# Kernel tuning notes

Measured on AMD Instinct MI355X. Metric: run time of the kernel, lower is better.

Reference implementation:

```python
import jax, jax.numpy as jnp
import numpy as np

LN_EPS = 1e-5
CLAMP = 1e-8


def _linear(x, W, b):
    return x @ W + b


def _layernorm(x, g, b):
    mu = x.mean(-1, keepdims=True)
    var = ((x - mu) ** 2).mean(-1, keepdims=True)
    return (x - mu) / jnp.sqrt(var + LN_EPS) * g + b


def _residual(x, W1, b1, W2, b2):
    return jax.nn.relu(_linear(jax.nn.relu(_linear(x, W1, b1)), W2, b2)) + x


def _forward(node_emb, attn_Wq, attn_bq, attn_Wk, attn_bk, attn_Wv, attn_bv,
             attn_Wd, attn_bd, attn_ln_g, attn_ln_b,
             mlp_r1_w1, mlp_r1_b1, mlp_r1_w2, mlp_r1_b2,
             mlp_r2_w1, mlp_r2_b1, mlp_r2_w2, mlp_r2_b2,
             mlp_out_w, mlp_out_b,
             log_phi_r0, log_phi_r1h, log_phi_r1v, log_phi_r2, r0_idx, n):
    x = node_emb  # [1, n^2, D]
    L = attn_Wq.shape[0]
    for l in range(L):  # mask in the original is all zeros -> plain softmax attention
        q = _linear(x, attn_Wq[l], attn_bq[l])
        k = _linear(x, attn_Wk[l], attn_bk[l])
        v = _linear(x, attn_Wv[l], attn_bv[l])
        probs = jax.nn.softmax(jnp.einsum('bqd,bkd->bqk', q, k), axis=-1)
        ctx = jnp.einsum('bqk,bkd->bqd', probs, v)
        x = _layernorm(_linear(ctx, attn_Wd[l], attn_bd[l]) + x, attn_ln_g[l], attn_ln_b[l])
    x0 = x[0]                                  # [n^2, D]
    feats = x0[r0_idx].reshape(r0_idx.shape[0], -1)  # [R0, 4D]
    h = _residual(feats, mlp_r1_w1, mlp_r1_b1, mlp_r1_w2, mlp_r1_b2)
    h = _residual(h, mlp_r2_w1, mlp_r2_b1, mlp_r2_w2, mlp_r2_b2)
    logits = _linear(h, mlp_out_w, mlp_out_b)  # [R0, 16]
    beliefs = jax.nn.softmax(logits, axis=-1).reshape(-1, 2, 2, 2, 2)

    m = n - 1  # plaquettes per row
    # --- R1 horizontal interior edges (row r in 1..n-2, col c in 0..n-2) ---
    r, c = np.meshgrid(np.arange(1, n - 1), np.arange(m), indexing='ij')
    above = ((r - 1) * m + c).ravel()
    below = (r * m + c).ravel()
    h_stack = jnp.stack([beliefs[above].sum((1, 2)),   # edge nodes at plaquette pos 2,3
                         beliefs[below].sum((3, 4))])  # edge nodes at plaquette pos 0,1
    h_bel = h_stack.mean(0)                            # [Eh,2,2]
    mism = jnp.sum((h_stack - h_bel) ** 2)
    # --- R1 vertical interior edges (row r in 0..n-2, col c in 1..n-2) ---
    r, c = np.meshgrid(np.arange(m), np.arange(1, n - 1), indexing='ij')
    left = (r * m + (c - 1)).ravel()
    right = (r * m + c).ravel()
    v_stack = jnp.stack([beliefs[left].sum((1, 3)),    # edge nodes at pos 1,3
                         beliefs[right].sum((2, 4))])  # edge nodes at pos 0,2
    v_bel = v_stack.mean(0)                            # [Ev,2,2]
    mism = mism + jnp.sum((v_stack - v_bel) ** 2)
    # --- R2 interior nodes (r, c in 1..n-2), parents are the 4 incident edges ---
    r, c = np.meshgrid(np.arange(1, n - 1), np.arange(1, n - 1), indexing='ij')
    hl = ((r - 1) * m + (c - 1)).ravel()
    hr = ((r - 1) * m + c).ravel()
    vu = ((r - 1) * (n - 2) + (c - 1)).ravel()
    vd = (r * (n - 2) + (c - 1)).ravel()
    n_stack = jnp.stack([h_bel[hl].sum(1), h_bel[hr].sum(2),
                         v_bel[vu].sum(1), v_bel[vd].sum(2)])
    n_bel = n_stack.mean(0)                            # [V,2]
    mism = mism + jnp.sum((n_stack - n_bel) ** 2)

    # --- Kikuchi energy: counts +1 (plaquette), -1 (edge), +1 (node); log_phi detached ---
    def reg_energy(b, lphi, cnt):
        bc = jnp.maximum(b, CLAMP)
        return cnt * jnp.sum(bc * (jnp.log(bc) - jax.lax.stop_gradient(lphi)))

    energy = (reg_energy(beliefs, log_phi_r0, 1.0)
              + reg_energy(h_bel, log_phi_r1h, -1.0)
              + reg_energy(v_bel, log_phi_r1v, -1.0)
              + reg_energy(n_bel, log_phi_r2, 1.0))
    return energy, mism


def setup_inputs() -> dict:
    n, D, L, HID, OUT = 64, 256, 2, 1024, 16
    m = n - 1
    R0, E, V = m * m, (n - 2) * m, (n - 2) * (n - 2)
    key = jax.random.key(0)
    ks = jax.random.split(key, 24)
    norm = lambda k, sh, s=0.05: jax.random.normal(k, sh, dtype=jnp.float32) * s
    r, c = np.meshgrid(np.arange(m), np.arange(m), indexing='ij')
    i = (r * n + c).ravel()
    r0_idx = jnp.asarray(np.stack([i, i + 1, i + n, i + n + 1], 1), dtype=jnp.int32)
    inp = {
        'node_emb': jax.random.normal(ks[0], (1, n * n, D), dtype=jnp.float32),
        'attn_Wq': norm(ks[1], (L, D, D)), 'attn_bq': jnp.zeros((L, D), jnp.float32),
        'attn_Wk': norm(ks[2], (L, D, D)), 'attn_bk': jnp.zeros((L, D), jnp.float32),
        'attn_Wv': norm(ks[3], (L, D, D)), 'attn_bv': jnp.zeros((L, D), jnp.float32),
        'attn_Wd': norm(ks[4], (L, D, D)), 'attn_bd': jnp.zeros((L, D), jnp.float32),
        'attn_ln_g': jnp.ones((L, D), jnp.float32), 'attn_ln_b': jnp.zeros((L, D), jnp.float32),
        'mlp_r1_w1': norm(ks[5], (HID, HID), 0.03), 'mlp_r1_b1': jnp.zeros((HID,), jnp.float32),
        'mlp_r1_w2': norm(ks[6], (HID, HID), 0.03), 'mlp_r1_b2': jnp.zeros((HID,), jnp.float32),
        'mlp_r2_w1': norm(ks[7], (HID, HID), 0.03), 'mlp_r2_b1': jnp.zeros((HID,), jnp.float32),
        'mlp_r2_w2': norm(ks[8], (HID, HID), 0.03), 'mlp_r2_b2': jnp.zeros((HID,), jnp.float32),
        'mlp_out_w': norm(ks[9], (HID, OUT), 0.03), 'mlp_out_b': jnp.zeros((OUT,), jnp.float32),
        'log_phi_r0': jax.random.normal(ks[10], (R0, 2, 2, 2, 2), dtype=jnp.float32),
        'log_phi_r1h': jax.random.normal(ks[11], (E, 2, 2), dtype=jnp.float32),
        'log_phi_r1v': jax.random.normal(ks[12], (E, 2, 2), dtype=jnp.float32),
        'log_phi_r2': jax.random.normal(ks[13], (V, 2), dtype=jnp.float32),
        'r0_idx': r0_idx,
        'n': n,
    }
    return inp


def reference(node_emb, attn_Wq, attn_bq, attn_Wk, attn_bk, attn_Wv, attn_bv,
              attn_Wd, attn_bd, attn_ln_g, attn_ln_b,
              mlp_r1_w1, mlp_r1_b1, mlp_r1_w2, mlp_r1_b2,
              mlp_r2_w1, mlp_r2_b1, mlp_r2_w2, mlp_r2_b2,
              mlp_out_w, mlp_out_b,
              log_phi_r0, log_phi_r1h, log_phi_r1v, log_phi_r2, r0_idx, n):
    return _forward(node_emb, attn_Wq, attn_bq, attn_Wk, attn_bk, attn_Wv, attn_bv,
                    attn_Wd, attn_bd, attn_ln_g, attn_ln_b,
                    mlp_r1_w1, mlp_r1_b1, mlp_r1_w2, mlp_r1_b2,
                    mlp_r2_w1, mlp_r2_b1, mlp_r2_w2, mlp_r2_b2,
                    mlp_out_w, mlp_out_b,
                    log_phi_r0, log_phi_r1h, log_phi_r1v, log_phi_r2, r0_idx, n)
```

## Files before the change

### kernel.cpp

```cpp
#include <hip/hip_runtime.h>
#include <hip/hip_bf16.h>
#include <math.h>

#define D_    256
#define NSQ   4096
#define NL    2
#define HID_  1024
#define R0_   3969
#define EH_   3906
#define EV_   3906
#define NV_   3844
#define LN_EPS_ 1e-5f
#define CLAMP_  1e-8f
#define TK_    64

typedef float f32x4 __attribute__((ext_vector_type(4)));
typedef __bf16 bf16x8 __attribute__((ext_vector_type(8)));
typedef unsigned short u16x8 __attribute__((ext_vector_type(8)));

__device__ __forceinline__ void gload_lds16(const void* g, void* l) {
    __builtin_amdgcn_global_load_lds(
        (const __attribute__((address_space(1))) void*)g,
        (__attribute__((address_space(3))) void*)l, 16, 0, 0);
}

template<int BM, int BN>
__device__ __forceinline__ void gemm_body(
    const __hip_bfloat16* __restrict__ A, const __hip_bfloat16* __restrict__ Bt,
    const float* __restrict__ bias,
    const float* __restrict__ resf, const __hip_bfloat16* __restrict__ resb,
    void* __restrict__ C, int M, int N, int K, int relu, int outmode,
    int bx, int by)
{
    constexpr int WR  = BM / 64;
    constexpr int WC  = 4 / WR;
    constexpr int WNT = BN / WC;
    constexpr int NF  = WNT / 16;
    constexpr int ACH = BM / 64;
    constexpr int BCH = BN / 64;
    constexpr int ASZ = BM * 32;

    __shared__ __hip_bfloat16 sm[2][(BM + BN) * 32];

    const int t = threadIdx.x;
    const int lane = t & 63, wave = t >> 6;
    const int ln = lane & 15, lg = lane >> 4;
    const int wr = (WR == 1) ? 0 : (wave >> 1);
    const int wc = (WR == 1) ? wave : (wave & 1);
    const int row0 = bx * BM, col0 = by * BN;

    int aoff[ACH], boff[BCH];
    #pragma unroll
    for (int c = 0; c < ACH; ++c) {
        int e = (c * 256 + t) * 8;
        int row = e >> 5, slot = (e >> 3) & 3;
        int kg = slot ^ (row & 3) ^ ((row >> 2) & 3);
        aoff[c] = row * K + kg * 8;
    }
    #pragma unroll
    for (int c = 0; c < BCH; ++c) {
        int e = (c * 256 + t) * 8;
        int row = e >> 5, slot = (e >> 3) & 3;
        int kg = slot ^ (row & 3) ^ ((row >> 2) & 3);
// ... 57 lines not shown
                    float v = acc[m][n][r] + bv;
                    if (relu) v = fmaxf(v, 0.f);
                    pk.h[r] = __float2bfloat16(v);
                }
                *(ushort4*)((__hip_bfloat16*)C + (size_t)col * M + rowb) = pk.u4;
            } else if (outmode == 3) {
                union { ushort4 u4; __hip_bfloat16 h[4]; } pk;
                #pragma unroll
                for (int r = 0; r < 4; ++r) {
                    float v = acc[m][n][r] + bv;
                    if (relu) v = fmaxf(v, 0.f);
                    pk.h[r] = __float2bfloat16(v);
                }
                size_t off = ((size_t)((rowb >> 5) * 16 + (col >> 4)) << 9)
                           + (size_t)(((rowb >> 3) & 3) * 16 + (col & 15)) * 8
                           + (rowb & 7);
                *(ushort4*)((__hip_bfloat16*)C + off) = pk.u4;
            } else {
                #pragma unroll
                for (int r = 0; r < 4; ++r) {
                    float v = acc[m][n][r] + bv;
                    if (relu) v = fmaxf(v, 0.f);
                    const size_t idx = (size_t)(rowb + r) * N + col;
                    if (resf) v += resf[idx];
                    if (resb) v += __bfloat162float(resb[idx]);
                    if (outmode == 0) ((float*)C)[idx] = v;
                    else ((__hip_bfloat16*)C)[idx] = __float2bfloat16(v);
                }
            }
        }
    }
}

template<int BM, int BN>
__global__ __launch_bounds__(256) void gemm_t(
    const __hip_bfloat16* __restrict__ A, const __hip_bfloat16* __restrict__ Bt,
    const float* __restrict__ bias,
    const float* __restrict__ resf, const __hip_bfloat16* __restrict__ resb,
    void* __restrict__ C, int M, int N, int K, int relu, int outmode)
{
    gemm_body<BM, BN>(A, Bt, bias, resf, resb, C, M, N, K, relu, outmode,
                      blockIdx.x, blockIdx.y);
}

__global__ __launch_bounds__(256) void gemm_qkv(
    const __hip_bfloat16* __restrict__ xb,
    const __hip_bfloat16* __restrict__ wqkt2, const __hip_bfloat16* __restrict__ wvt2,
    const float* __restrict__ bqk2, const float* __restrict__ bv,
    __hip_bfloat16* __restrict__ qkb, __hip_bfloat16* __restrict__ vf, int l)
{
    const __hip_bfloat16* Bt;
    const float* bias;
    void* C;
    int N, outmode, by;
    if (blockIdx.y < 4) {
        Bt = wqkt2 + (size_t)l * 131072; bias = bqk2 + l * 512;
        C = qkb; N = 512; outmode = 1; by = blockIdx.y;
    } else {
        Bt = wvt2 + (size_t)l * 65536; bias = bv + l * D_;
        C = vf; N = D_; outmode = 3; by = blockIdx.y - 4;
    }
    gemm_body<64, 128>(xb, Bt, bias, nullptr, nullptr, C, NSQ, N, D_, 0, outmode,
                       blockIdx.x, by);
}

__global__ __launch_bounds__(256, 2) void gemm_128p(
    const __hip_bfloat16* __restrict__ A, const __hip_bfloat16* __restrict__ Bt,
    const float* __restrict__ bias, const __hip_bfloat16* __restrict__ resb,
    __hip_bfloat16* __restrict__ C, int M, int N, int K, int relu)
{
    __shared__ __hip_bfloat16 sm[4][8192];

    const int t = threadIdx.x;
    const int lane = t & 63, wave = t >> 6;
    const int ln = lane & 15, lg = lane >> 4;
    const int wr = wave >> 1, wc = wave & 1;
    const int row0 = blockIdx.x * 128, col0 = blockIdx.y * 128;

    int aoff[2];
    #pragma unroll
    for (int c = 0; c < 2; ++c) {
        int e = (c * 256 + t) * 8;
        int row = e >> 5, slot = (e >> 3) & 3;
        int kg = slot ^ (row & 3) ^ ((row >> 2) & 3);
        aoff[c] = row * K + kg * 8;
    }
    const int sw = (ln & 3) ^ ((ln >> 2) & 3);

    const __hip_bfloat16* Ab = A + (size_t)row0 * K;
    const __hip_bfloat16* Bb = Bt + (size_t)col0 * K;

    f32x4 acc[4][4];
    #pragma unroll
    for (int m = 0; m < 4; ++m)
        #pragma unroll
        for (int n = 0; n < 4; ++n) acc[m][n] = f32x4{0.f, 0.f, 0.f, 0.f};

    auto STAGE = [&](int k0, int buf) {
        #pragma unroll
        for (int c = 0; c < 2; ++c) {
            gload_lds16(Ab + k0 + aoff[c], (char*)&sm[buf][0] + (c * 256 + t) * 16);
            gload_lds16(Bb + k0 + aoff[c], (char*)&sm[buf][4096] + (c * 256 + t) * 16);
        }
    };

    const int NT = K >> 5;
    STAGE(0, 0); STAGE(32, 1); STAGE(64, 2);

    for (int tt = 0; tt < NT; ++tt) {
        const int rem = NT - 1 - tt;
        if (rem >= 2)      asm volatile("s_waitcnt vmcnt(8)" ::: "memory");
        else if (rem == 1) asm volatile("s_waitcnt vmcnt(4)" ::: "memory");
        else               asm volatile("s_waitcnt vmcnt(0)" ::: "memory");
        __builtin_amdgcn_sched_barrier(0);
        __builtin_amdgcn_s_barrier();
        if (tt + 3 < NT) STAGE((tt + 3) * 32, (tt + 3) & 3);

        const char* base = (const char*)&sm[tt & 3][0];
        bf16x8 af[4], bfr[4];
        #pragma unroll
        for (int m = 0; m < 4; ++m)
            af[m] = *(const bf16x8*)(base +
                     (size_t)(wr * 64 + m * 16 + ln) * 64 + ((lg ^ sw) << 4));
        #pragma unroll
        for (int n = 0; n < 4; ++n)
            bfr[n] = *(const bf16x8*)(base + 8192 +
                     (size_t)(wc * 64 + n * 16 + ln) * 64 + ((lg ^ sw) << 4));
        #pragma unroll
        for (int m = 0; m < 4; ++m)
            #pragma unroll
            for (int n = 0; n < 4; ++n)
                acc[m][n] = __builtin_amdgcn_mfma_f32_16x16x32_bf16(
                    af[m], bfr[n], acc[m][n], 0, 0, 0);
    }

    #pragma unroll
    for (int m = 0; m < 4; ++m) {
        const int rowb = row0 + wr * 64 + m * 16 + lg * 4;
        #pragma unroll
        for (int n = 0; n < 4; ++n) {
            const int col = col0 + wc * 64 + n * 16 + ln;
            const float bv = bias[col];
            #pragma unroll
            for (int r = 0; r < 4; ++r) {
                float v = acc[m][n][r] + bv;
                if (relu) v = fmaxf(v, 0.f);
                const size_t idx = (size_t)(rowb + r) * N + col;
                if (resb) v += __bfloat162float(resb[idx]);
                C[idx] = __float2bfloat16(v);
            }
        }
    }
}

__global__ __launch_bounds__(256) void gemm_n16b(
    const __hip_bfloat16* __restrict__ A, const __hip_bfloat16* __restrict__ Bt,
    const float* __restrict__ bias, const float* __restrict__ lphi0,
    float* __restrict__ beliefs, float* __restrict__ out, int M, int K)
{
    const int t = threadIdx.x, lane = t & 63, wave = t >> 6;
    const int ln = lane & 15, lg = lane >> 4;
    const int r0 = blockIdx.x * 64 + wave * 16;
    f32x4 acc = {0.f, 0.f, 0.f, 0.f};
    for (int k0 = 0; k0 < K; k0 += 32) {
        bf16x8 a = *(const bf16x8*)(A + (size_t)(r0 + ln) * K + k0 + lg * 8);
        bf16x8 b = *(const bf16x8*)(Bt + (size_t)ln * K + k0 + lg * 8);
        acc = __builtin_amdgcn_mfma_f32_16x16x32_bf16(a, b, acc, 0, 0, 0);
    }
    float e = 0.f;
    #pragma unroll
    for (int r = 0; r < 4; ++r) {
        const int row = r0 + lg * 4 + r;
        float v = acc[r] + bias[ln];
        float mx = v;
        mx = fmaxf(mx, __shfl_xor(mx, 1));
        mx = fmaxf(mx, __shfl_xor(mx, 2));
        mx = fmaxf(mx, __shfl_xor(mx, 4));
        mx = fmaxf(mx, __shfl_xor(mx, 8));
        float ex = __expf(v - mx);
        float s = ex;
        s += __shfl_xor(s, 1);
        s += __shfl_xor(s, 2);
        s += __shfl_xor(s, 4);
        s += __shfl_xor(s, 8);
        if (row < R0_) {
            float bb = ex / s;
            beliefs[(size_t)row * 16 + ln] = bb;
            float bc = fmaxf(bb, CLAMP_);
            e += bc * (logf(bc) - lphi0[(size_t)row * 16 + ln]);
        }
    }
    #pragma unroll
    for (int off = 32; off; off >>= 1) e += __shfl_down(e, off);
    if (lane == 0) atomicAdd(&out[0], e);
}

__global__ __launch_bounds__(256) void prep_k(
    const float* __restrict__ node_emb, __hip_bfloat16* __restrict__ xb,
    const float* __restrict__ outw, __hip_bfloat16* __restrict__ outwt,
    const float* __restrict__ Wq, const float* __restrict__ Wk,
    const float* __restrict__ Wv, const float* __restrict__ Wd,
    __hip_bfloat16* __restrict__ wqkt2, __hip_bfloat16* __restrict__ wvt2,
    __hip_bfloat16* __restrict__ wdt2,
    const float* __restrict__ bq, const float* __restrict__ bk,
    float* __restrict__ bqk2,
    const float* __restrict__ M0, const float* __restrict__ M1,
    const float* __restrict__ M2, const float* __restrict__ M3,
    __hip_bfloat16* __restrict__ T0, __hip_bfloat16* __restrict__ T1,
    __hip_bfloat16* __restrict__ T2, __hip_bfloat16* __restrict__ T3,
    float* __restrict__ outp)
{
    __shared__ float tile[32][33];
    const int b = blockIdx.x, t = threadIdx.x;
    if (b == 0 && t < 2) outp[t] = 0.f;
    if (b < 1024) {
        int p = b * 256 + t;
        float4 v = *(const float4*)(node_emb + (size_t)p * 4);
        union { ushort4 u4; __hip_bfloat16 h[4]; } pk;
        pk.h[0] = __float2bfloat16(v.x); pk.h[1] = __float2bfloat16(v.y);
        pk.h[2] = __float2bfloat16(v.z); pk.h[3] = __float2bfloat16(v.w);
        *(ushort4*)(xb + (size_t)p * 4) = pk.u4;
    } else if (b < 1088) {
        int i = (b - 1024) * 256 + t;
        int n = i >> 10, k = i & 1023;
        outwt[i] = __float2bfloat16(outw[k * 16 + n]);
    } else if (b < 1600) {
        int idx = b - 1088;
// ... 6 lines not shown
                                    : wdt2 + (size_t)l * 65536;
        int k0 = bx * 32, n0 = by * 32;
        int r = t >> 3, c4 = (t & 7) * 4;
        float4 v = *(const float4*)(W + (size_t)(k0 + r) * 256 + n0 + c4);
        tile[r][c4 + 0] = v.x; tile[r][c4 + 1] = v.y;
        tile[r][c4 + 2] = v.z; tile[r][c4 + 3] = v.w;
        __syncthreads();
        union { ushort4 u4; __hip_bfloat16 h[4]; } pk;
        #pragma unroll
        for (int i = 0; i < 4; ++i) pk.h[i] = __float2bfloat16(tile[c4 + i][r]);
        *(ushort4*)(Wt + (size_t)(n0 + r) * 256 + k0 + c4) = pk.u4;
    } else if (b < 1604) {
        int idx = (b - 1600) * 256 + t;
        int l = idx >> 9, j = idx & 511;
        bqk2[idx] = j < 256 ? bq[l * 256 + j] : bk[l * 256 + j - 256];
    } else {
        int idx = b - 1604;
        int z = idx >> 10, rem = idx & 1023;
        const float* W = z == 0 ? M0 : z == 1 ? M1 : z == 2 ? M2 : M3;
        __hip_bfloat16* Wt = z == 0 ? T0 : z == 1 ? T1 : z == 2 ? T2 : T3;
        int k0 = (rem >> 5) * 32, n0 = (rem & 31) * 32;
        int r = t >> 3, c4 = (t & 7) * 4;
        float4 v = *(const float4*)(W + (size_t)(k0 + r) * 1024 + n0 + c4);
        tile[r][c4 + 0] = v.x; tile[r][c4 + 1] = v.y;
        tile[r][c4 + 2] = v.z; tile[r][c4 + 3] = v.w;
        __syncthreads();
        union { ushort4 u4; __hip_bfloat16 h[4]; } pk;
        #pragma unroll
        for (int i = 0; i < 4; ++i) pk.h[i] = __float2bfloat16(tile[c4 + i][r]);
        *(ushort4*)(Wt + (size_t)(n0 + r) * 1024 + k0 + c4) = pk.u4;
    }
}

template<int KS>
__global__ __launch_bounds__(512, 2) void attn_mfma_t(
    const __hip_bfloat16* __restrict__ qk, const __hip_bfloat16* __restrict__ vf,
    __hip_bfloat16* __restrict__ po, float* __restrict__ pm, float* __restrict__ pl)
{
    constexpr int KRANGE = NSQ / KS;
    constexpr int NT = KRANGE / TK_;
    constexpr int VOFF = 65536;
    constexpr int POFF = 98304;
    const int t = threadIdx.x;
    const int wave = t >> 6, lane = t & 63;
    const int ln = lane & 15, lg = lane >> 4;
    const int q0 = blockIdx.x * 128 + wave * 16;
    const int ks = blockIdx.y;
    const int k0 = ks * KRANGE;

    __shared__ __align__(16) char smem[116736];

    bf16x8 qa[8];
    #pragma unroll
    for (int s = 0; s < 8; ++s)
        qa[s] = *(const bf16x8*)(qk + (size_t)(q0 + ln) * 512 + s * 32 + lg * 8);

    int srcoff[4];
    #pragma unroll
    for (int c = 0; c < 4; ++c) {
        int row = c * 16 + (t >> 5);
        int g = (t & 31) ^ ((row & 15) << 1);
        srcoff[c] = row * 512 + 256 + g * 8;
    }
    int rb[8];
    #pragma unroll
    for (int s8 = 0; s8 < 8; ++s8)
        rb[s8] = ln * 512 + (((s8 * 4 + lg) ^ (ln << 1)) << 4);

    f32x4 o[16];
    #pragma unroll
    for (int nt = 0; nt < 16; ++nt) o[nt] = f32x4{0.f, 0.f, 0.f, 0.f};
// ... 85 lines not shown
        __builtin_amdgcn_s_barrier();
        const char* vl = smem + VOFF;
        #pragma unroll
        for (int ntd = 0; ntd < 16; ++ntd) {
            bf16x8 vb0 = *(const bf16x8*)(vl + ntd * 1024 + lane * 16);
            bf16x8 vb1 = *(const bf16x8*)(vl + 16384 + ntd * 1024 + lane * 16);
            o[ntd] = __builtin_amdgcn_mfma_f32_16x16x32_bf16(pa0, vb0, o[ntd], 0, 0, 0);
            o[ntd] = __builtin_amdgcn_mfma_f32_16x16x32_bf16(pa1, vb1, o[ntd], 0, 0, 0);
        }
        __syncthreads();
    }
    unsigned short* ob = (unsigned short*)(smem + wave * 8448);
    #pragma unroll
    for (int nt = 0; nt < 16; ++nt)
        #pragma unroll
        for (int r = 0; r < 4; ++r) {
            __hip_bfloat16 h = __float2bfloat16(o[nt][r]);
            ob[(lg * 4 + r) * 264 + nt * 16 + ln] = *(unsigned short*)&h;
        }
    asm volatile("s_waitcnt lgkmcnt(0)" ::: "memory");
    __builtin_amdgcn_sched_barrier(0);
    unsigned short* pob = (unsigned short*)po;
    #pragma unroll
    for (int i = 0; i < 8; ++i) {
        int f = i * 64 + lane;
        int row = f >> 5, dc = f & 31;
        u16x8 vv = *(const u16x8*)(ob + row * 264 + dc * 8);
        *(u16x8*)(pob + ((size_t)ks * NSQ + q0 + row) * D_ + dc * 8) = vv;
    }
    if (lane < 16) {
        pm[ks * NSQ + q0 + lane] = rm;
        pl[ks * NSQ + q0 + lane] = rl;
    }
}

template<int KS>
__global__ __launch_bounds__(256) void attn_combine_t(
    const __hip_bfloat16* __restrict__ po, const float* __restrict__ pm,
    const float* __restrict__ pl, __hip_bfloat16* __restrict__ ctx)
{
    const int idx8 = blockIdx.x * 256 + threadIdx.x;
    const int row = idx8 >> 5;
    float m[KS], ms = -1e30f;
    #pragma unroll
    for (int s = 0; s < KS; ++s) { m[s] = pm[s * NSQ + row]; ms = fmaxf(ms, m[s]); }
    float l = 0.f, w[KS];
    #pragma unroll
    for (int s = 0; s < KS; ++s) {
        w[s] = __expf(m[s] - ms);
        l += w[s] * pl[s * NSQ + row];
    }
    const float inv = 1.f / l;
    float num[8];
    #pragma unroll
    for (int j = 0; j < 8; ++j) num[j] = 0.f;
    #pragma unroll
    for (int s = 0; s < KS; ++s) {
        u16x8 v = *(const u16x8*)(po + (size_t)s * (NSQ * D_) + (size_t)idx8 * 8);
        #pragma unroll
        for (int j = 0; j < 8; ++j) {
            union { float f; unsigned u; } cv;
            cv.u = (unsigned)v[j] << 16;
            num[j] += w[s] * cv.f;
        }
    }
    union { u16x8 u8; __hip_bfloat16 h[8]; } pk;
    #pragma unroll
    for (int j = 0; j < 8; ++j) pk.h[j] = __float2bfloat16(num[j] * inv);
    *(u16x8*)(ctx + (size_t)idx8 * 8) = pk.u8;
}

__global__ __launch_bounds__(256) void ln_f32(
    const float* __restrict__ y, const float* __restrict__ g,
    const float* __restrict__ b, float* __restrict__ xo,
    __hip_bfloat16* __restrict__ xob, __hip_bfloat16* __restrict__ feats, int fin)
{
    const int lane = threadIdx.x & 63, wave = threadIdx.x >> 6;
    const int row = blockIdx.x * 4 + wave;
    float4 v = *(const float4*)(y + (size_t)row * D_ + lane * 4);
    float s = v.x + v.y + v.z + v.w;
    #pragma unroll
    for (int off = 1; off < 64; off <<= 1) s += __shfl_xor(s, off);
    float mu = s * (1.f / D_);
    float dx = v.x - mu, dy = v.y - mu, dz = v.z - mu, dw = v.w - mu;
    float q = dx * dx + dy * dy + dz * dz + dw * dw;
    #pragma unroll
    for (int off = 1; off < 64; off <<= 1) q += __shfl_xor(q, off);
    float inv = rsqrtf(q * (1.f / D_) + LN_EPS_);
    float4 gg = *(const float4*)(g + lane * 4);
    float4 bb = *(const float4*)(b + lane * 4);
    float4 o;
    o.x = dx * inv * gg.x + bb.x;
    o.y = dy * inv * gg.y + bb.y;
    o.z = dz * inv * gg.z + bb.z;
    o.w = dw * inv * gg.w + bb.w;
    union { ushort4 u4; __hip_bfloat16 h[4]; } pk;
    pk.h[0] = __float2bfloat16(o.x); pk.h[1] = __float2bfloat16(o.y);
    pk.h[2] = __float2bfloat16(o.z); pk.h[3] = __float2bfloat16(o.w);
    if (!fin) {
        *(float4*)(xo + (size_t)row * D_ + lane * 4) = o;
        *(ushort4*)(xob + (size_t)row * D_ + lane * 4) = pk.u4;
    } else {
        const int r = row >> 6, c = row & 63;
        if (r < 63 && c < 63)
            *(ushort4*)(feats + (size_t)(r * 63 + c) * 1024 + lane * 4) = pk.u4;
        if (r < 63 && c > 0)
            *(ushort4*)(feats + (size_t)(r * 63 + c - 1) * 1024 + 256 + lane * 4) = pk.u4;
        if (r > 0 && c < 63)
            *(ushort4*)(feats + (size_t)((r - 1) * 63 + c) * 1024 + 512 + lane * 4) = pk.u4;
        if (r > 0 && c > 0)
            *(ushort4*)(feats + (size_t)((r - 1) * 63 + c - 1) * 1024 + 768 + lane * 4) = pk.u4;
    }
}

__global__ __launch_bounds__(256) void edges_k(
    const float* __restrict__ beliefs, const float* __restrict__ lphih,
    const float* __restrict__ lphiv, float* __restrict__ hbel,
    float* __restrict__ vbel, float* __restrict__ out)
{
    int e = blockIdx.x * 256 + threadIdx.x;
    float el = 0.f, ml = 0.f;
    if (blockIdx.y == 0) {
        if (e < EH_) {
            const float* bA = beliefs + (size_t)e * 16;
            const float* bB = beliefs + (size_t)(e + 63) * 16;
            float s0[4] = {0,0,0,0}, s1[4] = {0,0,0,0};
            #pragma unroll
            for (int ab = 0; ab < 4; ++ab)
                #pragma unroll
                for (int cd = 0; cd < 4; ++cd) {
                    s0[cd] += bA[ab * 4 + cd];
                    s1[ab] += bB[ab * 4 + cd];
                }
            #pragma unroll
            for (int z = 0; z < 4; ++z) {
                float hb = 0.5f * (s0[z] + s1[z]);
                hbel[e * 4 + z] = hb;
                float d0 = s0[z] - hb, d1 = s1[z] - hb;
                ml += d0 * d0 + d1 * d1;
                float bc = fmaxf(hb, CLAMP_);
                el -= bc * (logf(bc) - lphih[e * 4 + z]);
            }
        }
    } else {
        if (e < EV_) {
            int r = e / 62, c = e % 62 + 1;
            const float* bL = beliefs + (size_t)(r * 63 + c - 1) * 16;
            const float* bR = beliefs + (size_t)(r * 63 + c) * 16;
            float s0[4] = {0,0,0,0}, s1[4] = {0,0,0,0};
            #pragma unroll
            for (int a = 0; a < 2; ++a)
                #pragma unroll
                for (int bq = 0; bq < 2; ++bq)
                    #pragma unroll
                    for (int c2 = 0; c2 < 2; ++c2)
                        #pragma unroll
                        for (int d = 0; d < 2; ++d) {
                            int idx = a * 8 + bq * 4 + c2 * 2 + d;
                            s0[bq * 2 + d]  += bL[idx];
                            s1[a * 2 + c2] += bR[idx];
                        }
            #pragma unroll
            for (int z = 0; z < 4; ++z) {
                float vb = 0.5f * (s0[z] + s1[z]);
                vbel[e * 4 + z] = vb;
                float d0 = s0[z] - vb, d1 = s1[z] - vb;
                ml += d0 * d0 + d1 * d1;
                float bc = fmaxf(vb, CLAMP_);
                el -= bc * (logf(bc) - lphiv[e * 4 + z]);
            }
        }
    }
    for (int off = 32; off; off >>= 1) { el += __shfl_down(el, off); ml += __shfl_down(ml, off); }
    if ((threadIdx.x & 63) == 0) { atomicAdd(&out[0], el); atomicAdd(&out[1], ml); }
}

__global__ __launch_bounds__(256) void node_k(
    const float* __restrict__ hbel, const float* __restrict__ vbel,
    const float* __restrict__ lphi2, float* __restrict__ out)
{
    int vtx = blockIdx.x * 256 + threadIdx.x;
    float el = 0.f, ml = 0.f;
    if (vtx < NV_) {
        int hl = (vtx / 62) * 63 + (vtx % 62);
        int hr = hl + 1;
        int vu = vtx;
        int vd = vtx + 62;
        float n0[2], n1[2], n2[2], n3[2];
        #pragma unroll
        for (int z = 0; z < 2; ++z) {
            n0[z] = hbel[hl * 4 + z] + hbel[hl * 4 + 2 + z];
            n1[z] = hbel[hr * 4 + z * 2] + hbel[hr * 4 + z * 2 + 1];
            n2[z] = vbel[vu * 4 + z] + vbel[vu * 4 + 2 + z];
            n3[z] = vbel[vd * 4 + z * 2] + vbel[vd * 4 + z * 2 + 1];
        }
        #pragma unroll
        for (int z = 0; z < 2; ++z) {
            float nb = 0.25f * (n0[z] + n1[z] + n2[z] + n3[z]);
            float d0 = n0[z] - nb, d1 = n1[z] - nb, d2 = n2[z] - nb, d3 = n3[z] - nb;
            ml += d0 * d0 + d1 * d1 + d2 * d2 + d3 * d3;
            float bc = fmaxf(nb, CLAMP_);
            el += bc * (logf(bc) - lphi2[vtx * 2 + z]);
        }
    }
    for (int off = 32; off; off >>= 1) { el += __shfl_down(el, off); ml += __shfl_down(ml, off); }
    if ((threadIdx.x & 63) == 0) { atomicAdd(&out[0], el); atomicAdd(&out[1], ml); }
}

extern "C" void kernel_launch(void* const* d_in, const int* in_sizes, int n_in,
                              void* d_out, int out_size, void* d_ws, size_t ws_size,
                              hipStream_t stream)
{
    (void)in_sizes; (void)n_in; (void)out_size; (void)ws_size;
    const float* node_emb = (const float*)d_in[0];
    const float* Wq  = (const float*)d_in[1];
    const float* bq  = (const float*)d_in[2];
    const float* Wk  = (const float*)d_in[3];
    const float* bk  = (const float*)d_in[4];
    const float* Wv  = (const float*)d_in[5];
    const float* bv  = (const float*)d_in[6];
    const float* Wd  = (const float*)d_in[7];
    const float* bd  = (const float*)d_in[8];
    const float* lng = (const float*)d_in[9];
    const float* lnb = (const float*)d_in[10];
    const float* r1w1 = (const float*)d_in[11];
    const float* r1b1 = (const float*)d_in[12];
    const float* r1w2 = (const float*)d_in[13];
    const float* r1b2 = (const float*)d_in[14];
    const float* r2w1 = (const float*)d_in[15];
    const float* r2b1 = (const float*)d_in[16];
    const float* r2w2 = (const float*)d_in[17];
    const float* r2b2 = (const float*)d_in[18];
    const float* outw = (const float*)d_in[19];
    const float* outb = (const float*)d_in[20];
    const float* lphi0 = (const float*)d_in[21];
    const float* lphih = (const float*)d_in[22];
    const float* lphiv = (const float*)d_in[23];
    const float* lphi2 = (const float*)d_in[24];

    float* ws = (float*)d_ws;
    float* x      = ws;
    __hip_bfloat16* xb = (__hip_bfloat16*)(ws + 1048576);
    float* belief = ws + 1638400;
    float* hbel   = ws + 1703936;
    float* vbel   = ws + 1720320;
    __hip_bfloat16* outwt = (__hip_bfloat16*)(ws + 1736704);
    float* arena  = ws + 1744896;

    __hip_bfloat16* wqkt2 = (__hip_bfloat16*)(arena);
    __hip_bfloat16* wvt2  = (__hip_bfloat16*)(arena + 131072);
    __hip_bfloat16* wdt2  = (__hip_bfloat16*)(arena + 196608);
    float* bqk2 = arena + 262144;
    __hip_bfloat16* qkb = (__hip_bfloat16*)(arena + 263168);
    __hip_bfloat16* vf  = (__hip_bfloat16*)(arena + 1311744);
    __hip_bfloat16* ctxb = vf;
    float* yb = arena + 1836032;
    float* pm = arena + 2884608;
    float* pl = arena + 2950144;
    __hip_bfloat16* po = (__hip_bfloat16*)(arena + 3015680);

    __hip_bfloat16* feats = (__hip_bfloat16*)(ws + 8954880);
    __hip_bfloat16* w1t = (__hip_bfloat16*)(ws + 11052032);
    __hip_bfloat16* w2t = (__hip_bfloat16*)(ws + 11576320);
    __hip_bfloat16* w3t = (__hip_bfloat16*)(ws + 12100608);
    __hip_bfloat16* w4t = (__hip_bfloat16*)(ws + 12624896);
    __hip_bfloat16* hA  = (__hip_bfloat16*)(arena);
    __hip_bfloat16* hB  = (__hip_bfloat16*)(arena + 2097152);

    float* outp = (float*)d_out;
    dim3 blk(256);
    dim3 blk512(512);
    prep_k<<<dim3(5700), blk, 0, stream>>>(node_emb, xb, outw, outwt,
                                           Wq, Wk, Wv, Wd, wqkt2, wvt2, wdt2,
                                           bq, bk, bqk2,
                                           r1w1, r1w2, r2w1, r2w2,
                                           w1t, w2t, w3t, w4t, outp);

    for (int l = 0; l < NL; ++l) {
        gemm_qkv<<<dim3(64, 6), blk, 0, stream>>>(xb, wqkt2, wvt2, bqk2, bv,
                                                  qkb, vf, l);
        attn_mfma_t<8><<<dim3(NSQ / 128, 8), blk512, 0, stream>>>(qkb, vf, po, pm, pl);
        attn_combine_t<8><<<dim3(NSQ * D_ / 2048), blk, 0, stream>>>(po, pm, pl, ctxb);
        gemm_t<64, 64><<<dim3(NSQ / 64, D_ / 64), blk, 0, stream>>>(
            ctxb, wdt2 + (size_t)l * 65536, bd + l * D_,
            (l == 0 ? node_emb : x), nullptr, yb, NSQ, D_, D_, 0, 0);
        ln_f32<<<dim3(NSQ / 4), blk, 0, stream>>>(yb, lng + l * D_, lnb + l * D_,
                                                  x, xb, feats, l);
    }

    dim3 gM(NSQ / 128, HID_ / 128);
    gemm_128p<<<gM, blk, 0, stream>>>(feats, w1t, r1b1, nullptr,
                                      hA, NSQ, HID_, HID_, 1);
    gemm_128p<<<gM, blk, 0, stream>>>(hA, w2t, r1b2, feats,
                                      hB, NSQ, HID_, HID_, 1);
    gemm_128p<<<gM, blk, 0, stream>>>(hB, w3t, r2b1, nullptr,
                                      hA, NSQ, HID_, HID_, 1);
    gemm_128p<<<gM, blk, 0, stream>>>(hA, w4t, r2b2, hB,
                                      feats, NSQ, HID_, HID_, 1);

    gemm_n16b<<<dim3(NSQ / 64), blk, 0, stream>>>(feats, outwt, outb, lphi0,
                                                  belief, outp, NSQ, HID_);
    edges_k<<<dim3((EH_ + 255) / 256, 2), blk, 0, stream>>>(belief, lphih, lphiv,
                                                            hbel, vbel, outp);
    node_k<<<dim3((NV_ + 255) / 256), blk, 0, stream>>>(hbel, vbel, lphi2, outp);
}
```

Baseline: 230.8 us.

## Merge attention, projection+LN and tail kernels using cooperative grid sync

Replaces several small back-to-back kernel launches with cooperative kernels that use grid-wide barriers: attention plus split-K combine, output projection plus layernorm, and the logits/edge/node tail. The aim is to cut launch gaps and inter-kernel drain time. In exchange, the grids are constrained to be co-resident, grid.sync costs something, and the LN stage now runs on only 256 blocks with 4 rows per wave.

```diff
diff --git a/kernel.cpp b/kernel.cpp
--- a/kernel.cpp
+++ b/kernel.cpp
@@ -1,6 +1,9 @@
 #include <hip/hip_runtime.h>
 #include <hip/hip_bf16.h>
+#include <hip/hip_cooperative_groups.h>
 #include <math.h>
+
+namespace cg = cooperative_groups;
 
 #define D_    256
 #define NSQ   4096
@@ -28,7 +31,7 @@
 __device__ __forceinline__ void gemm_body(
     const __hip_bfloat16* __restrict__ A, const __hip_bfloat16* __restrict__ Bt,
     const float* __restrict__ bias,
-    const float* __restrict__ resf, const __hip_bfloat16* __restrict__ resb,
+    const float* resf, const __hip_bfloat16* __restrict__ resb,
     void* __restrict__ C, int M, int N, int K, int relu, int outmode,
     int bx, int by)
 {
@@ -152,17 +155,6 @@
     }
 }
 
-template<int BM, int BN>
-__global__ __launch_bounds__(256) void gemm_t(
-    const __hip_bfloat16* __restrict__ A, const __hip_bfloat16* __restrict__ Bt,
-    const float* __restrict__ bias,
-    const float* __restrict__ resf, const __hip_bfloat16* __restrict__ resb,
-    void* __restrict__ C, int M, int N, int K, int relu, int outmode)
-{
-    gemm_body<BM, BN>(A, Bt, bias, resf, resb, C, M, N, K, relu, outmode,
-                      blockIdx.x, blockIdx.y);
-}
-
 __global__ __launch_bounds__(256) void gemm_qkv(
     const __hip_bfloat16* __restrict__ xb,
     const __hip_bfloat16* __restrict__ wqkt2, const __hip_bfloat16* __restrict__ wvt2,
@@ -184,6 +176,59 @@
                        blockIdx.x, by);
 }
 
+__global__ __launch_bounds__(256) void projln_k(
+    const __hip_bfloat16* __restrict__ ctxb, const __hip_bfloat16* __restrict__ wdt,
+    const float* __restrict__ bd, const float* resf,
+    float* __restrict__ yb,
+    const float* __restrict__ g, const float* __restrict__ b,
+    float* xo, __hip_bfloat16* __restrict__ xob,
+    __hip_bfloat16* __restrict__ feats, int fin)
+{
+    gemm_body<64, 64>(ctxb, wdt, bd, resf, nullptr, yb, NSQ, D_, D_, 0, 0,
+                      (int)(blockIdx.x & 63), (int)(blockIdx.x >> 6));
+    cg::this_grid().sync();
+
+    const int lane = threadIdx.x & 63, wave = threadIdx.x >> 6;
+    const int gw = blockIdx.x * 4 + wave;
+    for (int i = 0; i < 4; ++i) {
+        const int row = gw * 4 + i;
+        float4 v = *(const float4*)(yb + (size_t)row * D_ + lane * 4);
+        float s = v.x + v.y + v.z + v.w;
+        #pragma unroll
+        for (int off = 1; off < 64; off <<= 1) s += __shfl_xor(s, off);
+        float mu = s * (1.f / D_);
+        float dx = v.x - mu, dy = v.y - mu, dz = v.z - mu, dw = v.w - mu;
+        float q = dx * dx + dy * dy + dz * dz + dw * dw;
+        #pragma unroll
+        for (int off = 1; off < 64; off <<= 1) q += __shfl_xor(q, off);
+        float inv = rsqrtf(q * (1.f / D_) + LN_EPS_);
+        float4 gg = *(const float4*)(g + lane * 4);
+        float4 bb = *(const float4*)(b + lane * 4);
+        float4 o;
+        o.x = dx * inv * gg.x + bb.x;
+        o.y = dy * inv * gg.y + bb.y;
+        o.z = dz * inv * gg.z + bb.z;
+        o.w = dw * inv * gg.w + bb.w;
+        union { ushort4 u4; __hip_bfloat16 h[4]; } pk;
+        pk.h[0] = __float2bfloat16(o.x); pk.h[1] = __float2bfloat16(o.y);
+        pk.h[2] = __float2bfloat16(o.z); pk.h[3] = __float2bfloat16(o.w);
+        if (!fin) {
+            *(float4*)(xo + (size_t)row * D_ + lane * 4) = o;
+            *(ushort4*)(xob + (size_t)row * D_ + lane * 4) = pk.u4;
+        } else {
+            const int r = row >> 6, c = row & 63;
+            if (r < 63 && c < 63)
+                *(ushort4*)(feats + (size_t)(r * 63 + c) * 1024 + lane * 4) = pk.u4;
+            if (r < 63 && c > 0)
+                *(ushort4*)(feats + (size_t)(r * 63 + c - 1) * 1024 + 256 + lane * 4) = pk.u4;
+            if (r > 0 && c < 63)
+                *(ushort4*)(feats + (size_t)((r - 1) * 63 + c) * 1024 + 512 + lane * 4) = pk.u4;
+            if (r > 0 && c > 0)
+                *(ushort4*)(feats + (size_t)((r - 1) * 63 + c - 1) * 1024 + 768 + lane * 4) = pk.u4;
+        }
+    }
+}
+
 __global__ __launch_bounds__(256, 2) void gemm_128p(
     const __hip_bfloat16* __restrict__ A, const __hip_bfloat16* __restrict__ Bt,
     const float* __restrict__ bias, const __hip_bfloat16* __restrict__ resb,
@@ -271,48 +316,6 @@
             }
         }
     }
-}
-
-__global__ __launch_bounds__(256) void gemm_n16b(
-    const __hip_bfloat16* __restrict__ A, const __hip_bfloat16* __restrict__ Bt,
-    const float* __restrict__ bias, const float* __restrict__ lphi0,
-    float* __restrict__ beliefs, float* __restrict__ out, int M, int K)
-{
-    const int t = threadIdx.x, lane = t & 63, wave = t >> 6;
-    const int ln = lane & 15, lg = lane >> 4;
-    const int r0 = blockIdx.x * 64 + wave * 16;
-    f32x4 acc = {0.f, 0.f, 0.f, 0.f};
-    for (int k0 = 0; k0 < K; k0 += 32) {
-        bf16x8 a = *(const bf16x8*)(A + (size_t)(r0 + ln) * K + k0 + lg * 8);
-        bf16x8 b = *(const bf16x8*)(Bt + (size_t)ln * K + k0 + lg * 8);
-        acc = __builtin_amdgcn_mfma_f32_16x16x32_bf16(a, b, acc, 0, 0, 0);
-    }
-    float e = 0.f;
-    #pragma unroll
-    for (int r = 0; r < 4; ++r) {
-        const int row = r0 + lg * 4 + r;
-        float v = acc[r] + bias[ln];
-        float mx = v;
-        mx = fmaxf(mx, __shfl_xor(mx, 1));
-        mx = fmaxf(mx, __shfl_xor(mx, 2));
-        mx = fmaxf(mx, __shfl_xor(mx, 4));
-        mx = fmaxf(mx, __shfl_xor(mx, 8));
-        float ex = __expf(v - mx);
-        float s = ex;
-        s += __shfl_xor(s, 1);
-        s += __shfl_xor(s, 2);
-        s += __shfl_xor(s, 4);
-        s += __shfl_xor(s, 8);
-        if (row < R0_) {
-            float bb = ex / s;
-            beliefs[(size_t)row * 16 + ln] = bb;
-            float bc = fmaxf(bb, CLAMP_);
-            e += bc * (logf(bc) - lphi0[(size_t)row * 16 + ln]);
-        }
-    }
-    #pragma unroll
-    for (int off = 32; off; off >>= 1) e += __shfl_down(e, off);
-    if (lane == 0) atomicAdd(&out[0], e);
 }
 
 __global__ __launch_bounds__(256) void prep_k(
@@ -385,11 +388,12 @@
     }
 }
 
-template<int KS>
-__global__ __launch_bounds__(512, 2) void attn_mfma_t(
-    const __hip_bfloat16* __restrict__ qk, const __hip_bfloat16* __restrict__ vf,
-    __hip_bfloat16* __restrict__ po, float* __restrict__ pm, float* __restrict__ pl)
+__global__ __launch_bounds__(512, 2) void attn_fused(
+    const __hip_bfloat16* __restrict__ qk, const __hip_bfloat16* vf,
+    __hip_bfloat16* __restrict__ po, float* __restrict__ pm, float* __restrict__ pl,
+    __hip_bfloat16* ctx)
 {
+    constexpr int KS = 8;
     constexpr int KRANGE = NSQ / KS;
     constexpr int NT = KRANGE / TK_;
     constexpr int VOFF = 65536;
@@ -541,96 +545,94 @@
         pm[ks * NSQ + q0 + lane] = rm;
         pl[ks * NSQ + q0 + lane] = rl;
     }
+
+    cg::this_grid().sync();
+    {
+        const int bid = blockIdx.y * 32 + blockIdx.x;
+        const int idx8 = bid * 512 + t;
+        const int row = idx8 >> 5;
+        float m2[KS], ms = -1e30f;
+        #pragma unroll
+        for (int s = 0; s < KS; ++s) { m2[s] = pm[s * NSQ + row]; ms = fmaxf(ms, m2[s]); }
+        float l2 = 0.f, w2[KS];
+        #pragma unroll
+        for (int s = 0; s < KS; ++s) {
+            w2[s] = __expf(m2[s] - ms);
+            l2 += w2[s] * pl[s * NSQ + row];
+        }
+        const float inv = 1.f / l2;
+        float num[8];
+        #pragma unroll
+        for (int j = 0; j < 8; ++j) num[j] = 0.f;
+        #pragma unroll
+        for (int s = 0; s < KS; ++s) {
+            u16x8 v = *(const u16x8*)((const unsigned short*)po +
+                        (size_t)s * (NSQ * D_) + (size_t)idx8 * 8);
+            #pragma unroll
+            for (int j = 0; j < 8; ++j) {
+                union { float f; unsigned u; } cv;
+                cv.u = (unsigned)v[j] << 16;
+                num[j] += w2[s] * cv.f;
+            }
+        }
+        union { u16x8 u8; __hip_bfloat16 h[8]; } pk;
+        #pragma unroll
+        for (int j = 0; j < 8; ++j) pk.h[j] = __float2bfloat16(num[j] * inv);
+        *(u16x8*)(ctx + (size_t)idx8 * 8) = pk.u8;
+    }
 }
 
-template<int KS>
-__global__ __launch_bounds__(256) void attn_combine_t(
-    const __hip_bfloat16* __restrict__ po, const float* __restrict__ pm,
-    const float* __restrict__ pl, __hip_bfloat16* __restrict__ ctx)
+__global__ __launch_bounds__(256) void tail_k(
+    const __hip_bfloat16* __restrict__ A, const __hip_bfloat16* __restrict__ Bt,
+    const float* __restrict__ bias, const float* __restrict__ lphi0,
+    float* __restrict__ beliefs,
+    const float* __restrict__ lphih, const float* __restrict__ lphiv,
+    float* __restrict__ hbel, float* __restrict__ vbel,
+    const float* __restrict__ lphi2, float* __restrict__ out)
 {
-    const int idx8 = blockIdx.x * 256 + threadIdx.x;
-    const int row = idx8 >> 5;
-    float m[KS], ms = -1e30f;
-    #pragma unroll
-    for (int s = 0; s < KS; ++s) { m[s] = pm[s * NSQ + row]; ms = fmaxf(ms, m[s]); }
-    float l = 0.f, w[KS];
-    #pragma unroll
-    for (int s = 0; s < KS; ++s) {
-        w[s] = __expf(m[s] - ms);
-        l += w[s] * pl[s * NSQ + row];
-    }
-    const float inv = 1.f / l;
-    float num[8];
-    #pragma unroll
-    for (int j = 0; j < 8; ++j) num[j] = 0.f;
-    #pragma unroll
-    for (int s = 0; s < KS; ++s) {
-        u16x8 v = *(const u16x8*)(po + (size_t)s * (NSQ * D_) + (size_t)idx8 * 8);
-        #pragma unroll
-        for (int j = 0; j < 8; ++j) {
-            union { float f; unsigned u; } cv;
-            cv.u = (unsigned)v[j] << 16;
-            num[j] += w[s] * cv.f;
-        }
-    }
-    union { u16x8 u8; __hip_bfloat16 h[8]; } pk;
-    #pragma unroll
-    for (int j = 0; j < 8; ++j) pk.h[j] = __float2bfloat16(num[j] * inv);
-    *(u16x8*)(ctx + (size_t)idx8 * 8) = pk.u8;
-}
-
-__global__ __launch_bounds__(256) void ln_f32(
-    const float* __restrict__ y, const float* __restrict__ g,
-    const float* __restrict__ b, float* __restrict__ xo,
-    __hip_bfloat16* __restrict__ xob, __hip_bfloat16* __restrict__ feats, int fin)
-{
-    const int lane = threadIdx.x & 63, wave = threadIdx.x >> 6;
-    const int row = blockIdx.x * 4 + wave;
-    float4 v = *(const float4*)(y + (size_t)row * D_ + lane * 4);
-    float s = v.x + v.y + v.z + v.w;
-    #pragma unroll
-    for (int off = 1; off < 64; off <<= 1) s += __shfl_xor(s, off);
-    float mu = s * (1.f / D_);
-    float dx = v.x - mu, dy = v.y - mu, dz = v.z - mu, dw = v.w - mu;
-    float q = dx * dx + dy * dy + dz * dz + dw * dw;
-    #pragma unroll
-    for (int off = 1; off < 64; off <<= 1) q += __shfl_xor(q, off);
-    float inv = rsqrtf(q * (1.f / D_) + LN_EPS_);
-    float4 gg = *(const float4*)(g + lane * 4);
-    float4 bb = *(const float4*)(b + lane * 4);
-    float4 o;
-    o.x = dx * inv * gg.x + bb.x;
-    o.y = dy * inv * gg.y + bb.y;
-    o.z = dz * inv * gg.z + bb.z;
-    o.w = dw * inv * gg.w + bb.w;
-    union { ushort4 u4; __hip_bfloat16 h[4]; } pk;
-    pk.h[0] = __float2bfloat16(o.x); pk.h[1] = __float2bfloat16(o.y);
-    pk.h[2] = __float2bfloat16(o.z); pk.h[3] = __float2bfloat16(o.w);
-    if (!fin) {
-        *(float4*)(xo + (size_t)row * D_ + lane * 4) = o;
-        *(ushort4*)(xob + (size_t)row * D_ + lane * 4) = pk.u4;
-    } else {
-        const int r = row >> 6, c = row & 63;
-        if (r < 63 && c < 63)
-            *(ushort4*)(feats + (size_t)(r * 63 + c) * 1024 + lane * 4) = pk.u4;
-        if (r < 63 && c > 0)
-            *(ushort4*)(feats + (size_t)(r * 63 + c - 1) * 1024 + 256 + lane * 4) = pk.u4;
-        if (r > 0 && c < 63)
-            *(ushort4*)(feats + (size_t)((r - 1) * 63 + c) * 1024 + 512 + lane * 4) = pk.u4;
-        if (r > 0 && c > 0)
-            *(ushort4*)(feats + (size_t)((r - 1) * 63 + c - 1) * 1024 + 768 + lane * 4) = pk.u4;
-    }
-}
-
-__global__ __launch_bounds__(256) void edges_k(
-    const float* __restrict__ beliefs, const float* __restrict__ lphih,
-    const float* __restrict__ lphiv, float* __restrict__ hbel,
-    float* __restrict__ vbel, float* __restrict__ out)
-{
-    int e = blockIdx.x * 256 + threadIdx.x;
-    float el = 0.f, ml = 0.f;
-    if (blockIdx.y == 0) {
-        if (e < EH_) {
+    const int t = threadIdx.x, lane = t & 63, wave = t >> 6;
+    const int ln = lane & 15, lg = lane >> 4;
+    {
+        const int r0 = blockIdx.x * 64 + wave * 16;
+        f32x4 acc = {0.f, 0.f, 0.f, 0.f};
+        for (int k0 = 0; k0 < HID_; k0 += 32) {
+            bf16x8 a = *(const bf16x8*)(A + (size_t)(r0 + ln) * HID_ + k0 + lg * 8);
+            bf16x8 b = *(const bf16x8*)(Bt + (size_t)ln * HID_ + k0 + lg * 8);
+            acc = __builtin_amdgcn_mfma_f32_16x16x32_bf16(a, b, acc, 0, 0, 0);
+        }
+        float e = 0.f;
+        #pragma unroll
+        for (int r = 0; r < 4; ++r) {
+            const int row = r0 + lg * 4 + r;
+            float v = acc[r] + bias[ln];
+            float mx = v;
+            mx = fmaxf(mx, __shfl_xor(mx, 1));
+            mx = fmaxf(mx, __shfl_xor(mx, 2));
+            mx = fmaxf(mx, __shfl_xor(mx, 4));
+            mx = fmaxf(mx, __shfl_xor(mx, 8));
+            float ex = __expf(v - mx);
+            float s = ex;
+            s += __shfl_xor(s, 1);
+            s += __shfl_xor(s, 2);
+            s += __shfl_xor(s, 4);
+            s += __shfl_xor(s, 8);
+            if (row < R0_) {
+                float bb = ex / s;
+                beliefs[(size_t)row * 16 + ln] = bb;
+                float bc = fmaxf(bb, CLAMP_);
+                e += bc * (logf(bc) - lphi0[(size_t)row * 16 + ln]);
+            }
+        }
+        #pragma unroll
+        for (int off = 32; off; off >>= 1) e += __shfl_down(e, off);
+        if (lane == 0) atomicAdd(&out[0], e);
+    }
+    cg::this_grid().sync();
+    {
+        const int gg = blockIdx.x * 256 + t;
+        float el = 0.f, ml = 0.f;
+        if (gg < EH_) {
+            const int e = gg;
             const float* bA = beliefs + (size_t)e * 16;
             const float* bB = beliefs + (size_t)(e + 63) * 16;
             float s0[4] = {0,0,0,0}, s1[4] = {0,0,0,0};
@@ -650,9 +652,8 @@
                 float bc = fmaxf(hb, CLAMP_);
                 el -= bc * (logf(bc) - lphih[e * 4 + z]);
             }
-        }
-    } else {
-        if (e < EV_) {
+        } else if (gg >= 8192 && gg < 8192 + EV_) {
+            const int e = gg - 8192;
             int r = e / 62, c = e % 62 + 1;
             const float* bL = beliefs + (size_t)(r * 63 + c - 1) * 16;
             const float* bR = beliefs + (size_t)(r * 63 + c) * 16;
@@ -679,41 +680,40 @@
                 el -= bc * (logf(bc) - lphiv[e * 4 + z]);
             }
         }
-    }
-    for (int off = 32; off; off >>= 1) { el += __shfl_down(el, off); ml += __shfl_down(ml, off); }
-    if ((threadIdx.x & 63) == 0) { atomicAdd(&out[0], el); atomicAdd(&out[1], ml); }
-}
-
-__global__ __launch_bounds__(256) void node_k(
-    const float* __restrict__ hbel, const float* __restrict__ vbel,
-    const float* __restrict__ lphi2, float* __restrict__ out)
-{
-    int vtx = blockIdx.x * 256 + threadIdx.x;
-    float el = 0.f, ml = 0.f;
-    if (vtx < NV_) {
-        int hl = (vtx / 62) * 63 + (vtx % 62);
-        int hr = hl + 1;
-        int vu = vtx;
-        int vd = vtx + 62;
-        float n0[2], n1[2], n2[2], n3[2];
-        #pragma unroll
-        for (int z = 0; z < 2; ++z) {
-            n0[z] = hbel[hl * 4 + z] + hbel[hl * 4 + 2 + z];
-            n1[z] = hbel[hr * 4 + z * 2] + hbel[hr * 4 + z * 2 + 1];
-            n2[z] = vbel[vu * 4 + z] + vbel[vu * 4 + 2 + z];
-            n3[z] = vbel[vd * 4 + z * 2] + vbel[vd * 4 + z * 2 + 1];
-        }
-        #pragma unroll
-        for (int z = 0; z < 2; ++z) {
-            float nb = 0.25f * (n0[z] + n1[z] + n2[z] + n3[z]);
-            float d0 = n0[z] - nb, d1 = n1[z] - nb, d2 = n2[z] - nb, d3 = n3[z] - nb;
-            ml += d0 * d0 + d1 * d1 + d2 * d2 + d3 * d3;
-            float bc = fmaxf(nb, CLAMP_);
-            el += bc * (logf(bc) - lphi2[vtx * 2 + z]);
-        }
-    }
-    for (int off = 32; off; off >>= 1) { el += __shfl_down(el, off); ml += __shfl_down(ml, off); }
-    if ((threadIdx.x & 63) == 0) { atomicAdd(&out[0], el); atomicAdd(&out[1], ml); }
+        #pragma unroll
+        for (int off = 32; off; off >>= 1) { el += __shfl_down(el, off); ml += __shfl_down(ml, off); }
+        if (lane == 0) { atomicAdd(&out[0], el); atomicAdd(&out[1], ml); }
+    }
+    cg::this_grid().sync();
+    {
+        const int vtx = blockIdx.x * 256 + t;
+        float el = 0.f, ml = 0.f;
+        if (vtx < NV_) {
+            int hl = (vtx / 62) * 63 + (vtx % 62);
+            int hr = hl + 1;
+            int vu = vtx;
+            int vd = vtx + 62;
+            float n0[2], n1[2], n2[2], n3[2];
+            #pragma unroll
+            for (int z = 0; z < 2; ++z) {
+                n0[z] = hbel[hl * 4 + z] + hbel[hl * 4 + 2 + z];
+                n1[z] = hbel[hr * 4 + z * 2] + hbel[hr * 4 + z * 2 + 1];
+                n2[z] = vbel[vu * 4 + z] + vbel[vu * 4 + 2 + z];
+                n3[z] = vbel[vd * 4 + z * 2] + vbel[vd * 4 + z * 2 + 1];
+            }
+            #pragma unroll
+            for (int z = 0; z < 2; ++z) {
+                float nb = 0.25f * (n0[z] + n1[z] + n2[z] + n3[z]);
+                float d0 = n0[z] - nb, d1 = n1[z] - nb, d2 = n2[z] - nb, d3 = n3[z] - nb;
+                ml += d0 * d0 + d1 * d1 + d2 * d2 + d3 * d3;
+                float bc = fmaxf(nb, CLAMP_);
+                el += bc * (logf(bc) - lphi2[vtx * 2 + z]);
+            }
+        }
+        #pragma unroll
+        for (int off = 32; off; off >>= 1) { el += __shfl_down(el, off); ml += __shfl_down(ml, off); }
+        if (lane == 0) { atomicAdd(&out[0], el); atomicAdd(&out[1], ml); }
+    }
 }
 
 extern "C" void kernel_launch(void* const* d_in, const int* in_sizes, int n_in,
@@ -778,7 +778,6 @@
 
     float* outp = (float*)d_out;
     dim3 blk(256);
-    dim3 blk512(512);
     prep_k<<<dim3(5700), blk, 0, stream>>>(node_emb, xb, outw, outwt,
                                            Wq, Wk, Wv, Wd, wqkt2, wvt2, wdt2,
                                            bq, bk, bqk2,
@@ -788,13 +787,25 @@
     for (int l = 0; l < NL; ++l) {
         gemm_qkv<<<dim3(64, 6), blk, 0, stream>>>(xb, wqkt2, wvt2, bqk2, bv,
                                                   qkb, vf, l);
-        attn_mfma_t<8><<<dim3(NSQ / 128, 8), blk512, 0, stream>>>(qkb, vf, po, pm, pl);
-        attn_combine_t<8><<<dim3(NSQ * D_ / 2048), blk, 0, stream>>>(po, pm, pl, ctxb);
-        gemm_t<64, 64><<<dim3(NSQ / 64, D_ / 64), blk, 0, stream>>>(
-            ctxb, wdt2 + (size_t)l * 65536, bd + l * D_,
-            (l == 0 ? node_emb : x), nullptr, yb, NSQ, D_, D_, 0, 0);
-        ln_f32<<<dim3(NSQ / 4), blk, 0, stream>>>(yb, lng + l * D_, lnb + l * D_,
-                                                  x, xb, feats, l);
+        {
+            void* aArgs[] = {(void*)&qkb, (void*)&vf, (void*)&po,
+                             (void*)&pm, (void*)&pl, (void*)&ctxb};
+            hipLaunchCooperativeKernel((const void*)attn_fused,
+                                       dim3(NSQ / 128, 8), dim3(512), aArgs, 0, stream);
+        }
+        {
+            const __hip_bfloat16* wdtl = wdt2 + (size_t)l * 65536;
+            const float* bdl  = bd + l * D_;
+            const float* resl = (l == 0) ? node_emb : x;
+            const float* lngl = lng + l * D_;
+            const float* lnbl = lnb + l * D_;
+            int finl = l;
+            void* pArgs[] = {(void*)&ctxb, (void*)&wdtl, (void*)&bdl, (void*)&resl,
+                             (void*)&yb, (void*)&lngl, (void*)&lnbl,
+                             (void*)&x, (void*)&xb, (void*)&feats, (void*)&finl};
+            hipLaunchCooperativeKernel((const void*)projln_k,
+                                       dim3(256), dim3(256), pArgs, 0, stream);
+        }
     }
 
     dim3 gM(NSQ / 128, HID_ / 128);
@@ -807,9 +818,11 @@
     gemm_128p<<<gM, blk, 0, stream>>>(hA, w4t, r2b2, hB,
                                       feats, NSQ, HID_, HID_, 1);
 
-    gemm_n16b<<<dim3(NSQ / 64), blk, 0, stream>>>(feats, outwt, outb, lphi0,
-                                                  belief, outp, NSQ, HID_);
-    edges_k<<<dim3((EH_ + 255) / 256, 2), blk, 0, stream>>>(belief, lphih, lphiv,
-                                                            hbel, vbel, outp);
-    node_k<<<dim3((NV_ + 255) / 256), blk, 0, stream>>>(hbel, vbel, lphi2, outp);
+    {
+        void* tArgs[] = {(void*)&feats, (void*)&outwt, (void*)&outb, (void*)&lphi0,
+                         (void*)&belief, (void*)&lphih, (void*)&lphiv,
+                         (void*)&hbel, (void*)&vbel, (void*)&lphi2, (void*)&outp};
+        hipLaunchCooperativeKernel((const void*)tail_k,
+                                   dim3(64), dim3(256), tArgs, 0, stream);
+    }
 }
```

Result: slower. 436.0 us (+88.9%).

## Use BK=64 triple-buffered pipeline with 8-way XOR swizzle in gemm_128p

Applied to the files above, without the earlier changes.

The 128x128 GEMM K tile grows from 32 to 64, halving the number of barrier and waitcnt iterations. The ring drops from four 32-wide stages to three 64-wide stages, so prefetch depth falls from three tiles to two. The LDS swizzle becomes an 8-slot XOR over 128-byte rows to match the wider tile. LDS per block rises from 64KB to 96KB, which may limit two blocks per CU under the launch bounds.

```diff
diff --git a/kernel.cpp b/kernel.cpp
--- a/kernel.cpp
+++ b/kernel.cpp
@@ -189,7 +189,7 @@
     const float* __restrict__ bias, const __hip_bfloat16* __restrict__ resb,
     __hip_bfloat16* __restrict__ C, int M, int N, int K, int relu)
 {
-    __shared__ __hip_bfloat16 sm[4][8192];
+    __shared__ __hip_bfloat16 sm[3][16384];
 
     const int t = threadIdx.x;
     const int lane = t & 63, wave = t >> 6;
@@ -197,15 +197,14 @@
     const int wr = wave >> 1, wc = wave & 1;
     const int row0 = blockIdx.x * 128, col0 = blockIdx.y * 128;
 
-    int aoff[2];
-    #pragma unroll
-    for (int c = 0; c < 2; ++c) {
-        int e = (c * 256 + t) * 8;
-        int row = e >> 5, slot = (e >> 3) & 3;
-        int kg = slot ^ (row & 3) ^ ((row >> 2) & 3);
+    int aoff[4];
+    #pragma unroll
+    for (int c = 0; c < 4; ++c) {
+        int e = c * 256 + t;
+        int row = e >> 3, slot = e & 7;
+        int kg = slot ^ (row & 7);
         aoff[c] = row * K + kg * 8;
     }
-    const int sw = (ln & 3) ^ ((ln >> 2) & 3);
 
     const __hip_bfloat16* Ab = A + (size_t)row0 * K;
     const __hip_bfloat16* Bb = Bt + (size_t)col0 * K;
@@ -216,42 +215,51 @@
         #pragma unroll
         for (int n = 0; n < 4; ++n) acc[m][n] = f32x4{0.f, 0.f, 0.f, 0.f};
 
-    auto STAGE = [&](int k0, int buf) {
-        #pragma unroll
-        for (int c = 0; c < 2; ++c) {
+    auto STAGE = [&](int tile, int buf) {
+        const int k0 = tile * 64;
+        #pragma unroll
+        for (int c = 0; c < 4; ++c) {
             gload_lds16(Ab + k0 + aoff[c], (char*)&sm[buf][0] + (c * 256 + t) * 16);
-            gload_lds16(Bb + k0 + aoff[c], (char*)&sm[buf][4096] + (c * 256 + t) * 16);
+            gload_lds16(Bb + k0 + aoff[c], (char*)&sm[buf][8192] + (c * 256 + t) * 16);
         }
     };
 
-    const int NT = K >> 5;
-    STAGE(0, 0); STAGE(32, 1); STAGE(64, 2);
-
+    const int NT = K >> 6;
+    STAGE(0, 0); STAGE(1, 1);
+
+    int buf = 0;
     for (int tt = 0; tt < NT; ++tt) {
         const int rem = NT - 1 - tt;
-        if (rem >= 2)      asm volatile("s_waitcnt vmcnt(8)" ::: "memory");
-        else if (rem == 1) asm volatile("s_waitcnt vmcnt(4)" ::: "memory");
-        else               asm volatile("s_waitcnt vmcnt(0)" ::: "memory");
+        if (rem >= 1) asm volatile("s_waitcnt vmcnt(8)" ::: "memory");
+        else          asm volatile("s_waitcnt vmcnt(0)" ::: "memory");
         __builtin_amdgcn_sched_barrier(0);
         __builtin_amdgcn_s_barrier();
-        if (tt + 3 < NT) STAGE((tt + 3) * 32, (tt + 3) & 3);
-
-        const char* base = (const char*)&sm[tt & 3][0];
-        bf16x8 af[4], bfr[4];
-        #pragma unroll
-        for (int m = 0; m < 4; ++m)
-            af[m] = *(const bf16x8*)(base +
-                     (size_t)(wr * 64 + m * 16 + ln) * 64 + ((lg ^ sw) << 4));
-        #pragma unroll
-        for (int n = 0; n < 4; ++n)
-            bfr[n] = *(const bf16x8*)(base + 8192 +
-                     (size_t)(wc * 64 + n * 16 + ln) * 64 + ((lg ^ sw) << 4));
-        #pragma unroll
-        for (int m = 0; m < 4; ++m)
-            #pragma unroll
-            for (int n = 0; n < 4; ++n)
-                acc[m][n] = __builtin_amdgcn_mfma_f32_16x16x32_bf16(
-                    af[m], bfr[n], acc[m][n], 0, 0, 0);
+        if (tt + 2 < NT) STAGE(tt + 2, (buf + 2 >= 3) ? buf - 1 : buf + 2);
+
+        const char* base = (const char*)&sm[buf][0];
+        #pragma unroll
+        for (int kh = 0; kh < 2; ++kh) {
+            bf16x8 af[4], bfr[4];
+            #pragma unroll
+            for (int m = 0; m < 4; ++m) {
+                const int row = wr * 64 + m * 16 + ln;
+                af[m] = *(const bf16x8*)(base + row * 128 +
+                         (((kh * 4 + lg) ^ (row & 7)) << 4));
+            }
+            #pragma unroll
+            for (int n = 0; n < 4; ++n) {
+                const int row = wc * 64 + n * 16 + ln;
+                bfr[n] = *(const bf16x8*)(base + 16384 + row * 128 +
+                          (((kh * 4 + lg) ^ (row & 7)) << 4));
+            }
+            #pragma unroll
+            for (int m = 0; m < 4; ++m)
+                #pragma unroll
+                for (int n = 0; n < 4; ++n)
+                    acc[m][n] = __builtin_amdgcn_mfma_f32_16x16x32_bf16(
+                        af[m], bfr[n], acc[m][n], 0, 0, 0);
+        }
+        buf = (buf + 1 >= 3) ? 0 : buf + 1;
     }
 
     #pragma unroll
```

New measurement: 222.8 us. 1.04x faster.
